# Kernel tuning notes

Measured on AMD Instinct MI355X. Metric: run time of the kernel, lower is better.

The kernel has to match this reference:

```python
import jax, jax.numpy as jnp
import numpy as np

B = 64; H = 64; W = 64; C = 128
NH = 4; WS = 4; SHIFT = 2
N = WS * WS; HD = C // NH; SCALE = HD ** -0.5
HID = 4 * C; EPS = 1e-6


def _rel_index():
    # faithful to source: meshgrid(coords_w, coords_h, indexing='ij'); hard-coded 4 == WS
    coords = np.stack(np.meshgrid(np.arange(WS), np.arange(WS), indexing='ij')).reshape(2, -1)
    rel = coords[:, :, None] - coords[:, None, :]
    rel = rel.transpose(1, 2, 0).copy()
    rel[:, :, 0] += WS - 1
    rel[:, :, 1] += WS - 1
    rel[:, :, 0] *= 2 * WS - 1
    return rel.sum(-1)  # (N, N) int

REL_IDX = jnp.asarray(_rel_index())


def _attn_mask():
    img = np.zeros((H, W))
    sl = (slice(0, -WS), slice(-WS, -SHIFT), slice(-SHIFT, None))
    cnt = 0
    for hs in sl:
        for ws_ in sl:
            img[hs, ws_] = cnt
            cnt += 1
    mw = img.reshape(H // WS, WS, W // WS, WS).transpose(0, 2, 1, 3).reshape(-1, N)
    m = mw[:, None, :] - mw[:, :, None]  # (nW, N, N)
    return jnp.asarray(np.where(m != 0, -100.0, 0.0).astype(np.float32))

MASK = _attn_mask()  # (nW, N, N)


def _ln(x, s, b):
    mu = x.mean(-1, keepdims=True)
    var = ((x - mu) ** 2).mean(-1, keepdims=True)
    return (x - mu) * jax.lax.rsqrt(var + EPS) * s + b


def setup_inputs() -> dict:
    key = jax.random.key(0)
    ks = jax.random.split(key, 8)
    def nrm(k, shape, scale=0.02):
        return jax.random.normal(k, shape, jnp.float32) * scale
    return dict(
        x=jax.random.normal(ks[0], (B, H * W, C), jnp.float32),
        ln1_scale=jnp.ones((C,), jnp.float32), ln1_bias=jnp.zeros((C,), jnp.float32),
        qkv_w=nrm(ks[1], (C, 3 * C)), qkv_b=jnp.zeros((3 * C,), jnp.float32),
        rel_bias=nrm(ks[2], ((2 * WS - 1) ** 2, NH)),
        proj_w=nrm(ks[3], (C, C)), proj_b=jnp.zeros((C,), jnp.float32),
        ln2_scale=jnp.ones((C,), jnp.float32), ln2_bias=jnp.zeros((C,), jnp.float32),
        fc1_w=nrm(ks[4], (C, HID)), fc1_b=jnp.zeros((HID,), jnp.float32),
        fc2_w=nrm(ks[5], (HID, C)), fc2_b=jnp.zeros((C,), jnp.float32),
    )


def reference(x, ln1_scale, ln1_bias, qkv_w, qkv_b, rel_bias, proj_w, proj_b,
              ln2_scale, ln2_bias, fc1_w, fc1_b, fc2_w, fc2_b):
    shortcut = x
    h = _ln(x, ln1_scale, ln1_bias).reshape(B, H, W, C)
    h = jnp.roll(h, (-SHIFT, -SHIFT), axis=(1, 2))
    # window partition -> (B*nW, N, C)
    xw = h.reshape(B, H // WS, WS, W // WS, WS, C).transpose(0, 1, 3, 2, 4, 5).reshape(-1, N, C)
    B_ = xw.shape[0]
    qkv = (xw @ qkv_w + qkv_b).reshape(B_, N, 3, NH, HD).transpose(2, 0, 3, 1, 4)
    q, k, v = qkv[0] * SCALE, qkv[1], qkv[2]
    attn = jnp.einsum('bhnd,bhmd->bhnm', q, k)  # (B_, NH, N, N)
    bias = rel_bias[REL_IDX.reshape(-1)].reshape(N, N, NH).transpose(2, 0, 1)
    attn = attn + bias[None]
    nW = MASK.shape[0]
    attn = attn.reshape(B_ // nW, nW, NH, N, N) + MASK[None, :, None]
    attn = jax.nn.softmax(attn.reshape(B_, NH, N, N), axis=-1)
    attn = jax.nn.softmax(attn, axis=-1)  # source applies softmax twice when mask is present
    out = jnp.einsum('bhnm,bhmd->bhnd', attn, v).transpose(0, 2, 1, 3).reshape(B_, N, C)
    out = out @ proj_w + proj_b
    # window reverse
    h = out.reshape(B, H // WS, W // WS, WS, WS, C).transpose(0, 1, 3, 2, 4, 5).reshape(B, H, W, C)
    h = jnp.roll(h, (SHIFT, SHIFT), axis=(1, 2)).reshape(B, H * W, C)
    x = shortcut + h
    m = _ln(x, ln2_scale, ln2_bias)
    m = jax.nn.gelu(m @ fc1_w + fc1_b) @ fc2_w + fc2_b  # flax nn.gelu default approximate=True
    return x + m
```

## Files before the change

### kernel.cpp

```cpp
#include <hip/hip_runtime.h>

typedef __bf16 bf16x8 __attribute__((ext_vector_type(8)));
typedef __bf16 bf16x4 __attribute__((ext_vector_type(4)));
typedef float f32x4 __attribute__((ext_vector_type(4)));
typedef unsigned short us8 __attribute__((ext_vector_type(8)));
typedef unsigned short us4 __attribute__((ext_vector_type(4)));
typedef short sh4 __attribute__((ext_vector_type(4)));

#define SCALE_Q 0.17677669529663687f

__device__ __forceinline__ unsigned short f2b(float f) {
    __bf16 h = (__bf16)f;
    return __builtin_bit_cast(unsigned short, h);
}
__device__ __forceinline__ float b2f(unsigned short h) {
    union { unsigned u; float f; } v; v.u = ((unsigned)h) << 16;
    return v.f;
}
__device__ __forceinline__ f32x4 mfma16(us8 a, us8 b, f32x4 c) {
    return __builtin_amdgcn_mfma_f32_16x16x32_bf16(
        __builtin_bit_cast(bf16x8, a), __builtin_bit_cast(bf16x8, b), c, 0, 0, 0);
}

#if __has_builtin(__builtin_amdgcn_mfma_f32_16x16x16bf16_1k)
__device__ __forceinline__ f32x4 mfma16k16(us4 a, us4 b, f32x4 c) {
    return __builtin_amdgcn_mfma_f32_16x16x16bf16_1k(
        __builtin_bit_cast(sh4, a), __builtin_bit_cast(sh4, b), c, 0, 0, 0);
}
#elif __has_builtin(__builtin_amdgcn_mfma_f32_16x16x16_bf16)
__device__ __forceinline__ f32x4 mfma16k16(us4 a, us4 b, f32x4 c) {
    return __builtin_amdgcn_mfma_f32_16x16x16_bf16(
        __builtin_bit_cast(bf16x4, a), __builtin_bit_cast(bf16x4, b), c, 0, 0, 0);
}
#else
__device__ __forceinline__ f32x4 mfma16k16(us4 a, us4 b, f32x4 c) {
    asm volatile("v_mfma_f32_16x16x16_bf16 %0, %1, %2, %0"
                 : "+v"(c) : "v"(a), "v"(b));
    return c;
}
#endif

__device__ __forceinline__ us8 lds_ld8(const unsigned short* base, int byteoff) {
    return *(const us8*)((const char*)base + byteoff);
}
__device__ __forceinline__ void lds_st8(unsigned short* base, int byteoff, us8 v) {
    *(us8*)((char*)base + byteoff) = v;
}

__global__ void k_pack_qkvw(const float* __restrict__ qkv_w, unsigned short* __restrict__ dst) {
    int gid = blockIdx.x * 256 + threadIdx.x;
    int blk = gid >> 9, rem = gid & 511;
    int lane = rem >> 3, j = rem & 7;
    int w = blk / 24, r1 = blk % 24, ct = r1 >> 2, kk = r1 & 3;
    int col = w * 96 + ct * 16 + (lane & 15);
    int k = kk * 32 + (lane >> 4) * 8 + j;
    float v = qkv_w[k * 384 + col];
    if (col < 128) v *= SCALE_Q;
    dst[gid] = f2b(v);
}
__global__ void k_scale_qkvb(const float* __restrict__ qkv_b, float* __restrict__ dst) {
    int i = blockIdx.x * 256 + threadIdx.x;
    if (i < 384) dst[i] = qkv_b[i] * (i < 128 ? SCALE_Q : 1.f);
}
__global__ void k_pack_projw(const float* __restrict__ proj_w, unsigned short* __restrict__ dst) {
    int gid = blockIdx.x * 256 + threadIdx.x;
    int blk = gid >> 9, rem = gid & 511;
    int lane = rem >> 3, j = rem & 7;
    int w = blk >> 3, r1 = blk & 7, ct = r1 >> 2, kk = r1 & 3;
    int col = w * 32 + ct * 16 + (lane & 15);
    int k = kk * 32 + (lane >> 4) * 8 + j;
    dst[gid] = f2b(proj_w[k * 128 + col]);
}

__global__ void k_pack_mlp(const float* __restrict__ fc1_w, const float* __restrict__ fc2_w,
                           unsigned short* __restrict__ wPack) {
    int gid = blockIdx.x * 256 + threadIdx.x;
    int pair = gid >> 13;
    int rem = gid & 8191;
    float v;
    if (rem < 4096) {
        int half = rem >> 11;
        int r2 = rem & 2047;
        int kk = r2 >> 9, r3 = r2 & 511;
        int lane = r3 >> 3, j = r3 & 7;
        int m = lane & 15;
        int col = pair * 32 + (m >> 2) * 8 + half * 4 + (m & 3);
        int k = kk * 32 + (lane >> 4) * 8 + j;
        v = fc1_w[(size_t)k * 512 + col];
    } else {
        int r2 = rem - 4096;
        int co = r2 >> 9, r3 = r2 & 511;
        int lane = r3 >> 3, j = r3 & 7;
        int k = pair * 32 + (lane >> 4) * 8 + j;
        v = fc2_w[(size_t)k * 128 + co * 16 + (lane & 15)];
    }
    wPack[gid] = f2b(v);
}

__global__ __launch_bounds__(256, 3) void k_block1(
    const float* __restrict__ x,
    const float* __restrict__ ln1s, const float* __restrict__ ln1b,
    const unsigned short* __restrict__ qkvWp, const float* __restrict__ qkvBs,
    const float* __restrict__ relb,
    const unsigned short* __restrict__ projWp, const float* __restrict__ projB,
    float* __restrict__ out)
{
    __shared__ unsigned short sm[4 * 6144];
    __shared__ float sbias[196];
    const int tid = threadIdx.x;
    const int wave = tid >> 6, lane = tid & 63;
    const int g = lane >> 4, m16 = lane & 15;
    if (tid < 196) sbias[tid] = relb[tid];
    const int win0 = blockIdx.x * 4;
    const int winM = win0 + wave;
    const int bbM = winM >> 8, whM = (winM >> 4) & 15, wnM = winM & 15;

    {
        float4 sc0 = *(const float4*)(ln1s + m16 * 8);
        float4 sc1 = *(const float4*)(ln1s + m16 * 8 + 4);
        float4 bi0 = *(const float4*)(ln1b + m16 * 8);
        float4 bi1 = *(const float4*)(ln1b + m16 * 8 + 4);
        #pragma unroll
        for (int it = 0; it < 4; ++it) {
            int tok = it * 4 + g;
            int ti = tok >> 2, tj = tok & 3;
            int hh = (whM * 4 + ti + 2) & 63, ww = (wnM * 4 + tj + 2) & 63;
            const float* xr = x + ((((size_t)bbM << 12) | (hh << 6) | ww) * 128) + m16 * 8;
            float4 v0 = *(const float4*)xr, v1 = *(const float4*)(xr + 4);
            float sum = v0.x + v0.y + v0.z + v0.w + v1.x + v1.y + v1.z + v1.w;
            float sq  = v0.x*v0.x + v0.y*v0.y + v0.z*v0.z + v0.w*v0.w
                      + v1.x*v1.x + v1.y*v1.y + v1.z*v1.z + v1.w*v1.w;
            #pragma unroll
            for (int m = 1; m < 16; m <<= 1) { sum += __shfl_xor(sum, m); sq += __shfl_xor(sq, m); }
            float mu = sum * 0.0078125f;
            float rstd = rsqrtf(sq * 0.0078125f - mu * mu + 1e-6f);
            us8 o;
            o[0] = f2b((v0.x - mu) * rstd * sc0.x + bi0.x);
            o[1] = f2b((v0.y - mu) * rstd * sc0.y + bi0.y);
            o[2] = f2b((v0.z - mu) * rstd * sc0.z + bi0.z);
            o[3] = f2b((v0.w - mu) * rstd * sc0.w + bi0.w);
            o[4] = f2b((v1.x - mu) * rstd * sc1.x + bi1.x);
            o[5] = f2b((v1.y - mu) * rstd * sc1.y + bi1.y);
            o[6] = f2b((v1.z - mu) * rstd * sc1.z + bi1.z);
            o[7] = f2b((v1.w - mu) * rstd * sc1.w + bi1.w);
            lds_st8(sm, wave * 12288 + tok * 256 + ((m16 * 16) ^ ((tok & 7) << 4)), o);
        }
    }
    __syncthreads();

    us8 afr[4][4];
    #pragma unroll
    for (int w = 0; w < 4; ++w)
        #pragma unroll
        for (int k = 0; k < 4; ++k)
            afr[w][k] = lds_ld8(sm, w * 12288 + m16 * 256 + ((k * 64 + g * 16) ^ ((m16 & 7) << 4)));
    __syncthreads();

    #pragma unroll
    for (int ct = 0; ct < 6; ++ct) {
        const unsigned short* bp = qkvWp + (size_t)((wave * 6 + ct) * 4) * 512 + lane * 8;
        us8 b0 = *(const us8*)(bp);
        us8 b1 = *(const us8*)(bp + 512);
        us8 b2 = *(const us8*)(bp + 1024);
        us8 b3 = *(const us8*)(bp + 1536);
        f32x4 acc[4] = {{0.f,0.f,0.f,0.f},{0.f,0.f,0.f,0.f},{0.f,0.f,0.f,0.f},{0.f,0.f,0.f,0.f}};
        #pragma unroll
        for (int w = 0; w < 4; ++w) {
            acc[w] = mfma16(afr[w][0], b0, acc[w]);
            acc[w] = mfma16(afr[w][1], b1, acc[w]);
            acc[w] = mfma16(afr[w][2], b2, acc[w]);
            acc[w] = mfma16(afr[w][3], b3, acc[w]);
        }
        const int c = wave * 96 + ct * 16 + m16;
        const float bias = qkvBs[c];
        const int s = c >> 7;
        const int rem = c & 127, hq = rem >> 5, hd = rem & 31;
        #pragma unroll
        for (int w = 0; w < 4; ++w) {
            const int base = w * 12288;
            if (s == 2) {
                us4 pk;
                #pragma unroll
                for (int jj = 0; jj < 4; ++jj) pk[jj] = f2b(acc[w][jj] + bias);
                *(us4*)((char*)sm + base + 8192 + hq * 1024 + hd * 32
                        + ((g ^ ((hd >> 2) & 3)) << 3)) = pk;
            } else {
                #pragma unroll
                for (int jj = 0; jj < 4; ++jj) {
                    int tok = g * 4 + jj;
                    int chunk = (hd >> 3) ^ ((tok >> 1) & 3);
                    *(unsigned short*)((char*)sm + base + s * 4096 + hq * 1024
                                       + tok * 64 + chunk * 16 + (hd & 7) * 2)
                        = f2b(acc[w][jj] + bias);
                }
            }
        }
    }
    __syncthreads();

    {
        const int base = wave * 12288;
        const int ti = m16 >> 2, tj = m16 & 3;
        const int hhq = whM * 4 + ti, wwq = wnM * 4 + tj;
        const int myid = (hhq < 60 ? 0 : (hhq < 62 ? 3 : 6)) + (wwq < 60 ? 0 : (wwq < 62 ? 1 : 2));
        const int qkswz = (g ^ ((m16 >> 1) & 3)) * 16;
        const int vswz  = (g ^ ((m16 >> 2) & 3)) << 3;
        f32x4 po[4][2];
        #pragma unroll
        for (int h = 0; h < 4; ++h) {
            us8 kf = lds_ld8(sm, base + 4096 + h * 1024 + m16 * 64 + qkswz);
            us8 qf = lds_ld8(sm, base +        h * 1024 + m16 * 64 + qkswz);
            f32x4 st = mfma16(kf, qf, (f32x4){0.f,0.f,0.f,0.f});
            float p[4];
            #pragma unroll
            for (int jj = 0; jj < 4; ++jj) {
                int kk = g * 4 + jj;
                int pi = kk >> 2, pj = kk & 3;
                int hhk = whM * 4 + pi, wwk = wnM * 4 + pj;
                int pid = (hhk < 60 ? 0 : (hhk < 62 ? 3 : 6)) + (wwk < 60 ? 0 : (wwk < 62 ? 1 : 2));
                float v = st[jj] + sbias[((ti - pi + 3) * 7 + (tj - pj + 3)) * 4 + h];
                p[jj] = (pid != myid) ? v - 100.f : v;
            }
            #pragma unroll
            for (int rep = 0; rep < 2; ++rep) {
                float mx = fmaxf(fmaxf(p[0], p[1]), fmaxf(p[2], p[3]));
                mx = fmaxf(mx, __shfl_xor(mx, 16));
                mx = fmaxf(mx, __shfl_xor(mx, 32));
                float ssum = 0.f;
                #pragma unroll
                for (int jj = 0; jj < 4; ++jj) { p[jj] = __expf(p[jj] - mx); ssum += p[jj]; }
                ssum += __shfl_xor(ssum, 16);
                ssum += __shfl_xor(ssum, 32);
                float inv = 1.f / ssum;
                #pragma unroll
                for (int jj = 0; jj < 4; ++jj) p[jj] *= inv;
            }
            us4 pf;
            #pragma unroll
            for (int jj = 0; jj < 4; ++jj) pf[jj] = f2b(p[jj]);
            #pragma unroll
            for (int dh = 0; dh < 2; ++dh) {
                us4 vf = *(const us4*)((const char*)sm + base + 8192 + h * 1024
                                       + (dh * 16 + m16) * 32 + vswz);
                po[h][dh] = mfma16k16(vf, pf, (f32x4){0.f,0.f,0.f,0.f});
            }
        }
        #pragma unroll
        for (int h = 0; h < 4; ++h)
            #pragma unroll
            for (int dh = 0; dh < 2; ++dh) {
                us4 pk;
                #pragma unroll
                for (int jj = 0; jj < 4; ++jj) pk[jj] = f2b(po[h][dh][jj]);
                *(us4*)((char*)sm + base + m16 * 256
                        + ((h * 64 + dh * 32 + g * 8) ^ ((m16 & 7) << 4))) = pk;
            }
    }
    __syncthreads();

    {
        us8 cfr[4][4];
        #pragma unroll
        for (int w = 0; w < 4; ++w)
            #pragma unroll
            for (int k = 0; k < 4; ++k)
                cfr[w][k] = lds_ld8(sm, w * 12288 + m16 * 256 + ((k * 64 + g * 16) ^ ((m16 & 7) << 4)));
        #pragma unroll
        for (int ct = 0; ct < 2; ++ct) {
            const unsigned short* bp = projWp + (size_t)((wave * 2 + ct) * 4) * 512 + lane * 8;
            us8 b0 = *(const us8*)(bp);
            us8 b1 = *(const us8*)(bp + 512);
            us8 b2 = *(const us8*)(bp + 1024);
            us8 b3 = *(const us8*)(bp + 1536);
            const int c = wave * 32 + ct * 16 + m16;
            const float pb = projB[c];
            #pragma unroll
            for (int w = 0; w < 4; ++w) {
                f32x4 acc = {0.f, 0.f, 0.f, 0.f};
                acc = mfma16(cfr[w][0], b0, acc);
                acc = mfma16(cfr[w][1], b1, acc);
                acc = mfma16(cfr[w][2], b2, acc);
                acc = mfma16(cfr[w][3], b3, acc);
                const int winw = win0 + w;
                const int bb = winw >> 8, wh = (winw >> 4) & 15, wn = winw & 15;
                #pragma unroll
                for (int jj = 0; jj < 4; ++jj) {
                    int tok = g * 4 + jj;
                    int hh3 = (wh * 4 + (tok >> 2) + 2) & 63;
                    int ww3 = (wn * 4 + (tok & 3) + 2) & 63;
                    size_t t = (((size_t)bb << 12) | (hh3 << 6) | ww3);
                    out[t * 128 + c] = acc[jj] + pb + x[t * 128 + c];
                }
            }
        }
    }
}

__global__ __launch_bounds__(512, 4) void k_block2(
    float* __restrict__ out,
    const float* __restrict__ ln2s, const float* __restrict__ ln2b,
    const unsigned short* __restrict__ wPack,
    const float* __restrict__ fc1B, const float* __restrict__ fc2B)
{
    __shared__ unsigned short smem[16384];
    const int tid = threadIdx.x;
    const int wave = tid >> 6, lane = tid & 63;
    const int g = lane >> 4, m16 = lane & 15;
    const size_t r0 = (size_t)blockIdx.x * 128;
    unsigned short* scr = &smem[wave * 2048];

    {
        float4 sc0 = *(const float4*)(ln2s + m16 * 8);
        float4 sc1 = *(const float4*)(ln2s + m16 * 8 + 4);
        float4 bi0 = *(const float4*)(ln2b + m16 * 8);
        float4 bi1 = *(const float4*)(ln2b + m16 * 8 + 4);
        #pragma unroll
        for (int it = 0; it < 4; ++it) {
            int lr = it * 4 + g;
            const float* xr = out + (r0 + wave * 16 + lr) * 128 + m16 * 8;
            float4 v0 = *(const float4*)xr, v1 = *(const float4*)(xr + 4);
            float sum = v0.x + v0.y + v0.z + v0.w + v1.x + v1.y + v1.z + v1.w;
            float sq  = v0.x*v0.x + v0.y*v0.y + v0.z*v0.z + v0.w*v0.w
                      + v1.x*v1.x + v1.y*v1.y + v1.z*v1.z + v1.w*v1.w;
            #pragma unroll
            for (int m = 1; m < 16; m <<= 1) { sum += __shfl_xor(sum, m); sq += __shfl_xor(sq, m); }
            float mu = sum * 0.0078125f;
            float rstd = rsqrtf(sq * 0.0078125f - mu * mu + 1e-6f);
            us8 o;
            o[0] = f2b((v0.x - mu) * rstd * sc0.x + bi0.x);
            o[1] = f2b((v0.y - mu) * rstd * sc0.y + bi0.y);
            o[2] = f2b((v0.z - mu) * rstd * sc0.z + bi0.z);
            o[3] = f2b((v0.w - mu) * rstd * sc0.w + bi0.w);
            o[4] = f2b((v1.x - mu) * rstd * sc1.x + bi1.x);
            o[5] = f2b((v1.y - mu) * rstd * sc1.y + bi1.y);
            o[6] = f2b((v1.z - mu) * rstd * sc1.z + bi1.z);
            o[7] = f2b((v1.w - mu) * rstd * sc1.w + bi1.w);
            lds_st8(scr, lr * 256 + ((m16 * 16) ^ ((lr & 7) << 4)), o);
        }
    }
    us8 bx[4];
    #pragma unroll
    for (int kk = 0; kk < 4; ++kk)
        bx[kk] = lds_ld8(scr, m16 * 256 + ((kk * 64 + g * 16) ^ ((m16 & 7) << 4)));
    __syncthreads();

    #pragma unroll
    for (int sub = 0; sub < 2; ++sub) {
        const unsigned short* src = wPack + sub * 4096 + tid * 8;
        unsigned short* dst = &smem[sub * 4096 + wave * 512];
#if __has_builtin(__builtin_amdgcn_global_load_lds)
        __builtin_amdgcn_global_load_lds(
            (const __attribute__((address_space(1))) void*)src,
            (__attribute__((address_space(3))) void*)dst, 16, 0, 0);
#else
        *(us8*)(dst + lane * 8) = *(const us8*)src;
#endif
    }
    __syncthreads();

    f32x4 accO[8];
    #pragma unroll
    for (int co = 0; co < 8; ++co) accO[co] = (f32x4){0.f, 0.f, 0.f, 0.f};

    for (int p = 0; p < 16; ++p) {
        if (p < 15) {
            #pragma unroll
            for (int sub = 0; sub < 2; ++sub) {
                const unsigned short* src = wPack + (p + 1) * 8192 + sub * 4096 + tid * 8;
                unsigned short* dst = &smem[((p + 1) & 1) * 8192 + sub * 4096 + wave * 512];
#if __has_builtin(__builtin_amdgcn_global_load_lds)
                __builtin_amdgcn_global_load_lds(
                    (const __attribute__((address_space(1))) void*)src,
                    (__attribute__((address_space(3))) void*)dst, 16, 0, 0);
#else
                *(us8*)(dst + lane * 8) = *(const us8*)src;
#endif
            }
        }
        const char* wb = (const char*)&smem[(p & 1) * 8192];
        f32x4 hA = {0.f, 0.f, 0.f, 0.f};
        hA = mfma16(*(const us8*)(wb +    0 + lane * 16), bx[0], hA);
        hA = mfma16(*(const us8*)(wb + 1024 + lane * 16), bx[1], hA);
        hA = mfma16(*(const us8*)(wb + 2048 + lane * 16), bx[2], hA);
        hA = mfma16(*(const us8*)(wb + 3072 + lane * 16), bx[3], hA);
        f32x4 hB = {0.f, 0.f, 0.f, 0.f};
        hB = mfma16(*(const us8*)(wb + 4096 + lane * 16), bx[0], hB);
        hB = mfma16(*(const us8*)(wb + 5120 + lane * 16), bx[1], hB);
        hB = mfma16(*(const us8*)(wb + 6144 + lane * 16), bx[2], hB);
        hB = mfma16(*(const us8*)(wb + 7168 + lane * 16), bx[3], hB);
        float4 bA = *(const float4*)(fc1B + p * 32 + g * 8);
        float4 bB = *(const float4*)(fc1B + p * 32 + g * 8 + 4);
        us8 pa;
        #pragma unroll
        for (int jj = 0; jj < 4; ++jj) {
            float v = hA[jj] + ((const float*)&bA)[jj];
            float z = v + 0.044715f * v * v * v;
            float e = __builtin_amdgcn_exp2f(-2.3022082f * z);
            pa[jj] = f2b(v * __builtin_amdgcn_rcpf(1.f + e));
            float w = hB[jj] + ((const float*)&bB)[jj];
            float z2 = w + 0.044715f * w * w * w;
            float e2 = __builtin_amdgcn_exp2f(-2.3022082f * z2);
            pa[4 + jj] = f2b(w * __builtin_amdgcn_rcpf(1.f + e2));
        }
        #pragma unroll
        for (int co = 0; co < 8; ++co) {
            us8 bw = *(const us8*)(wb + 8192 + co * 1024 + lane * 16);
            accO[co] = mfma16(pa, bw, accO[co]);
        }
        __syncthreads();
    }

    #pragma unroll
    for (int co = 0; co < 8; ++co) {
        int col = co * 16 + m16;
        float b2v = fc2B[col];
        #pragma unroll
        for (int jj = 0; jj < 4; ++jj) {
            size_t row = r0 + wave * 16 + g * 4 + jj;
            float* op = out + row * 128 + col;
            *op = accO[co][jj] + b2v + *op;
        }
    }
}

extern "C" void kernel_launch(void* const* d_in, const int* in_sizes, int n_in,
                              void* d_out, int out_size, void* d_ws, size_t ws_size,
                              hipStream_t stream) {
    const float* x        = (const float*)d_in[0];
    const float* ln1_s    = (const float*)d_in[1];
    const float* ln1_b    = (const float*)d_in[2];
    const float* qkv_w    = (const float*)d_in[3];
    const float* qkv_b    = (const float*)d_in[4];
    const float* rel_bias = (const float*)d_in[5];
    const float* proj_w   = (const float*)d_in[6];
    const float* proj_b   = (const float*)d_in[7];
    const float* ln2_s    = (const float*)d_in[8];
    const float* ln2_b    = (const float*)d_in[9];
    const float* fc1_w    = (const float*)d_in[10];
    const float* fc1_b    = (const float*)d_in[11];
    const float* fc2_w    = (const float*)d_in[12];
    const float* fc2_b    = (const float*)d_in[13];
    float* out = (float*)d_out;
    char* ws = (char*)d_ws;

    unsigned short* qkv_wp  = (unsigned short*)(ws);
    unsigned short* proj_wp = (unsigned short*)(ws + 98304);
    unsigned short* wpack   = (unsigned short*)(ws + 131072);
    float*          qkv_bs  = (float*)(ws + 393216);

    k_pack_qkvw<<<192, 256, 0, stream>>>(qkv_w, qkv_wp);
    k_scale_qkvb<<<2, 256, 0, stream>>>(qkv_b, qkv_bs);
    k_pack_projw<<<64, 256, 0, stream>>>(proj_w, proj_wp);
    k_pack_mlp<<<512, 256, 0, stream>>>(fc1_w, fc2_w, wpack);

    k_block1<<<4096, 256, 0, stream>>>(x, ln1_s, ln1_b, qkv_wp, qkv_bs, rel_bias,
                                       proj_wp, proj_b, out);
    k_block2<<<2048, 512, 0, stream>>>(out, ln2_s, ln2_b, wpack, fc1_b, fc2_b);
}
```

Baseline: 223.5 us.

## Give each MLP wave two row tiles so weight LDS loads are reused

The MLP kernel now runs 4 waves per block instead of 8, and each wave handles 32 rows, two 16-row tiles, rather than 16. Each fc1/fc2 weight fragment read from LDS now feeds two MFMAs, halving LDS weight traffic per FLOP. The first weight chunk's load is issued before LayerNorm so the global-to-LDS copy overlaps with it. In exchange each wave holds twice the accumulators and activations, so register pressure rises. The launch bounds are lowered to 3 blocks of 256 threads, which with 48KB of LDS per block can reduce occupancy.

New measurement: 216.5 us. 3.2% less time.

```diff
diff --git a/kernel.cpp b/kernel.cpp
--- a/kernel.cpp
+++ b/kernel.cpp
@@ -296,28 +296,43 @@
     }
 }
 
-__global__ __launch_bounds__(512, 4) void k_block2(
+__global__ __launch_bounds__(256, 3) void k_block2(
     float* __restrict__ out,
     const float* __restrict__ ln2s, const float* __restrict__ ln2b,
     const unsigned short* __restrict__ wPack,
     const float* __restrict__ fc1B, const float* __restrict__ fc2B)
 {
-    __shared__ unsigned short smem[16384];
+    __shared__ unsigned short smem[24576];
     const int tid = threadIdx.x;
     const int wave = tid >> 6, lane = tid & 63;
     const int g = lane >> 4, m16 = lane & 15;
     const size_t r0 = (size_t)blockIdx.x * 128;
     unsigned short* scr = &smem[wave * 2048];
 
-    {
-        float4 sc0 = *(const float4*)(ln2s + m16 * 8);
-        float4 sc1 = *(const float4*)(ln2s + m16 * 8 + 4);
-        float4 bi0 = *(const float4*)(ln2b + m16 * 8);
-        float4 bi1 = *(const float4*)(ln2b + m16 * 8 + 4);
+    #pragma unroll
+    for (int sub = 0; sub < 4; ++sub) {
+        const unsigned short* src = wPack + sub * 2048 + tid * 8;
+        unsigned short* dst = &smem[8192 + sub * 2048 + wave * 512];
+#if __has_builtin(__builtin_amdgcn_global_load_lds)
+        __builtin_amdgcn_global_load_lds(
+            (const __attribute__((address_space(1))) void*)src,
+            (__attribute__((address_space(3))) void*)dst, 16, 0, 0);
+#else
+        *(us8*)(dst + lane * 8) = *(const us8*)src;
+#endif
+    }
+
+    float4 sc0 = *(const float4*)(ln2s + m16 * 8);
+    float4 sc1 = *(const float4*)(ln2s + m16 * 8 + 4);
+    float4 bi0 = *(const float4*)(ln2b + m16 * 8);
+    float4 bi1 = *(const float4*)(ln2b + m16 * 8 + 4);
+    us8 bx[2][4];
+    #pragma unroll
+    for (int rt = 0; rt < 2; ++rt) {
         #pragma unroll
         for (int it = 0; it < 4; ++it) {
             int lr = it * 4 + g;
-            const float* xr = out + (r0 + wave * 16 + lr) * 128 + m16 * 8;
+            const float* xr = out + (r0 + wave * 32 + rt * 16 + lr) * 128 + m16 * 8;
             float4 v0 = *(const float4*)xr, v1 = *(const float4*)(xr + 4);
             float sum = v0.x + v0.y + v0.z + v0.w + v1.x + v1.y + v1.z + v1.w;
             float sq  = v0.x*v0.x + v0.y*v0.y + v0.z*v0.z + v0.w*v0.w
@@ -337,37 +352,24 @@
             o[7] = f2b((v1.w - mu) * rstd * sc1.w + bi1.w);
             lds_st8(scr, lr * 256 + ((m16 * 16) ^ ((lr & 7) << 4)), o);
         }
-    }
-    us8 bx[4];
-    #pragma unroll
-    for (int kk = 0; kk < 4; ++kk)
-        bx[kk] = lds_ld8(scr, m16 * 256 + ((kk * 64 + g * 16) ^ ((m16 & 7) << 4)));
+        #pragma unroll
+        for (int kk = 0; kk < 4; ++kk)
+            bx[rt][kk] = lds_ld8(scr, m16 * 256 + ((kk * 64 + g * 16) ^ ((m16 & 7) << 4)));
+    }
     __syncthreads();
 
-    #pragma unroll
-    for (int sub = 0; sub < 2; ++sub) {
-        const unsigned short* src = wPack + sub * 4096 + tid * 8;
-        unsigned short* dst = &smem[sub * 4096 + wave * 512];
-#if __has_builtin(__builtin_amdgcn_global_load_lds)
-        __builtin_amdgcn_global_load_lds(
-            (const __attribute__((address_space(1))) void*)src,
-            (__attribute__((address_space(3))) void*)dst, 16, 0, 0);
-#else
-        *(us8*)(dst + lane * 8) = *(const us8*)src;
-#endif
-    }
-    __syncthreads();
-
-    f32x4 accO[8];
-    #pragma unroll
-    for (int co = 0; co < 8; ++co) accO[co] = (f32x4){0.f, 0.f, 0.f, 0.f};
+    f32x4 accO[2][8];
+    #pragma unroll
+    for (int rt = 0; rt < 2; ++rt)
+        #pragma unroll
+        for (int co = 0; co < 8; ++co) accO[rt][co] = (f32x4){0.f, 0.f, 0.f, 0.f};
 
     for (int p = 0; p < 16; ++p) {
         if (p < 15) {
             #pragma unroll
-            for (int sub = 0; sub < 2; ++sub) {
-                const unsigned short* src = wPack + (p + 1) * 8192 + sub * 4096 + tid * 8;
-                unsigned short* dst = &smem[((p + 1) & 1) * 8192 + sub * 4096 + wave * 512];
+            for (int sub = 0; sub < 4; ++sub) {
+                const unsigned short* src = wPack + (p + 1) * 8192 + sub * 2048 + tid * 8;
+                unsigned short* dst = &smem[8192 + ((p + 1) & 1) * 8192 + sub * 2048 + wave * 512];
 #if __has_builtin(__builtin_amdgcn_global_load_lds)
                 __builtin_amdgcn_global_load_lds(
                     (const __attribute__((address_space(1))) void*)src,
@@ -377,50 +379,61 @@
 #endif
             }
         }
-        const char* wb = (const char*)&smem[(p & 1) * 8192];
-        f32x4 hA = {0.f, 0.f, 0.f, 0.f};
-        hA = mfma16(*(const us8*)(wb +    0 + lane * 16), bx[0], hA);
-        hA = mfma16(*(const us8*)(wb + 1024 + lane * 16), bx[1], hA);
-        hA = mfma16(*(const us8*)(wb + 2048 + lane * 16), bx[2], hA);
-        hA = mfma16(*(const us8*)(wb + 3072 + lane * 16), bx[3], hA);
-        f32x4 hB = {0.f, 0.f, 0.f, 0.f};
-        hB = mfma16(*(const us8*)(wb + 4096 + lane * 16), bx[0], hB);
-        hB = mfma16(*(const us8*)(wb + 5120 + lane * 16), bx[1], hB);
-        hB = mfma16(*(const us8*)(wb + 6144 + lane * 16), bx[2], hB);
-        hB = mfma16(*(const us8*)(wb + 7168 + lane * 16), bx[3], hB);
+        const char* wb = (const char*)&smem[8192 + (p & 1) * 8192];
+        f32x4 hA0 = {0.f,0.f,0.f,0.f}, hA1 = {0.f,0.f,0.f,0.f};
+        #pragma unroll
+        for (int kk = 0; kk < 4; ++kk) {
+            us8 aw = *(const us8*)(wb + kk * 1024 + lane * 16);
+            hA0 = mfma16(aw, bx[0][kk], hA0);
+            hA1 = mfma16(aw, bx[1][kk], hA1);
+        }
+        f32x4 hB0 = {0.f,0.f,0.f,0.f}, hB1 = {0.f,0.f,0.f,0.f};
+        #pragma unroll
+        for (int kk = 0; kk < 4; ++kk) {
+            us8 aw = *(const us8*)(wb + 4096 + kk * 1024 + lane * 16);
+            hB0 = mfma16(aw, bx[0][kk], hB0);
+            hB1 = mfma16(aw, bx[1][kk], hB1);
+        }
         float4 bA = *(const float4*)(fc1B + p * 32 + g * 8);
         float4 bB = *(const float4*)(fc1B + p * 32 + g * 8 + 4);
-        us8 pa;
+        us8 pa0, pa1;
         #pragma unroll
         for (int jj = 0; jj < 4; ++jj) {
-            float v = hA[jj] + ((const float*)&bA)[jj];
-            float z = v + 0.044715f * v * v * v;
-            float e = __builtin_amdgcn_exp2f(-2.3022082f * z);
-            pa[jj] = f2b(v * __builtin_amdgcn_rcpf(1.f + e));
-            float w = hB[jj] + ((const float*)&bB)[jj];
-            float z2 = w + 0.044715f * w * w * w;
-            float e2 = __builtin_amdgcn_exp2f(-2.3022082f * z2);
-            pa[4 + jj] = f2b(w * __builtin_amdgcn_rcpf(1.f + e2));
+            float v0 = hA0[jj] + ((const float*)&bA)[jj];
+            float z0 = v0 + 0.044715f * v0 * v0 * v0;
+            pa0[jj] = f2b(v0 * __builtin_amdgcn_rcpf(1.f + __builtin_amdgcn_exp2f(-2.3022082f * z0)));
+            float w0 = hB0[jj] + ((const float*)&bB)[jj];
+            float y0 = w0 + 0.044715f * w0 * w0 * w0;
+            pa0[4 + jj] = f2b(w0 * __builtin_amdgcn_rcpf(1.f + __builtin_amdgcn_exp2f(-2.3022082f * y0)));
+            float v1 = hA1[jj] + ((const float*)&bA)[jj];
+            float z1 = v1 + 0.044715f * v1 * v1 * v1;
+            pa1[jj] = f2b(v1 * __builtin_amdgcn_rcpf(1.f + __builtin_amdgcn_exp2f(-2.3022082f * z1)));
+            float w1 = hB1[jj] + ((const float*)&bB)[jj];
+            float y1 = w1 + 0.044715f * w1 * w1 * w1;
+            pa1[4 + jj] = f2b(w1 * __builtin_amdgcn_rcpf(1.f + __builtin_amdgcn_exp2f(-2.3022082f * y1)));
         }
         #pragma unroll
         for (int co = 0; co < 8; ++co) {
             us8 bw = *(const us8*)(wb + 8192 + co * 1024 + lane * 16);
-            accO[co] = mfma16(pa, bw, accO[co]);
+            accO[0][co] = mfma16(pa0, bw, accO[0][co]);
+            accO[1][co] = mfma16(pa1, bw, accO[1][co]);
         }
         __syncthreads();
     }
 
     #pragma unroll
-    for (int co = 0; co < 8; ++co) {
-        int col = co * 16 + m16;
-        float b2v = fc2B[col];
-        #pragma unroll
-        for (int jj = 0; jj < 4; ++jj) {
-            size_t row = r0 + wave * 16 + g * 4 + jj;
-            float* op = out + row * 128 + col;
-            *op = accO[co][jj] + b2v + *op;
-        }
-    }
+    for (int rt = 0; rt < 2; ++rt)
+        #pragma unroll
+        for (int co = 0; co < 8; ++co) {
+            int col = co * 16 + m16;
+            float b2v = fc2B[col];
+            #pragma unroll
+            for (int jj = 0; jj < 4; ++jj) {
+                size_t row = r0 + wave * 32 + rt * 16 + g * 4 + jj;
+                float* op = out + row * 128 + col;
+                *op = accO[rt][co][jj] + b2v + *op;
+            }
+        }
 }
 
 extern "C" void kernel_launch(void* const* d_in, const int* in_sizes, int n_in,
@@ -455,5 +468,5 @@
 
     k_block1<<<4096, 256, 0, stream>>>(x, ln1_s, ln1_b, qkv_wp, qkv_bs, rel_bias,
                                        proj_wp, proj_b, out);
-    k_block2<<<2048, 512, 0, stream>>>(out, ln2_s, ln2_b, wpack, fc1_b, fc2_b);
-}
+    k_block2<<<2048, 256, 0, stream>>>(out, ln2_s, ln2_b, wpack, fc1_b, fc2_b);
+}
```

## Fuse attention block and MLP block into one kernel via LDS handoff

Applied to the files above, without the earlier changes.

Merges the attention/projection kernel and the LN2+MLP kernel into a single kernel. The post-attention residual stays in shared memory, so it is no longer written to global memory and read back by a second kernel. The cost is a larger shared-memory footprint, launch bounds lowered from 3 to 2 blocks, and MLP weight streaming now done per 64-token block (256 threads) instead of per 128-token block. That doubles the total weight loads from global or L2 and may reduce occupancy.

After: 267.2 us. +19.5%, slower.

```diff
diff --git a/kernel.cpp b/kernel.cpp
--- a/kernel.cpp
+++ b/kernel.cpp
@@ -97,16 +97,20 @@
     wPack[gid] = f2b(v);
 }
 
-__global__ __launch_bounds__(256, 3) void k_block1(
+__global__ __launch_bounds__(256, 2) void k_fused(
     const float* __restrict__ x,
     const float* __restrict__ ln1s, const float* __restrict__ ln1b,
     const unsigned short* __restrict__ qkvWp, const float* __restrict__ qkvBs,
     const float* __restrict__ relb,
     const unsigned short* __restrict__ projWp, const float* __restrict__ projB,
+    const float* __restrict__ ln2s, const float* __restrict__ ln2b,
+    const unsigned short* __restrict__ wPack,
+    const float* __restrict__ fc1B, const float* __restrict__ fc2B,
     float* __restrict__ out)
 {
-    __shared__ unsigned short sm[4 * 6144];
+    __shared__ unsigned short smem[32768];
     __shared__ float sbias[196];
+    unsigned short* sm = smem;
     const int tid = threadIdx.x;
     const int wave = tid >> 6, lane = tid & 63;
     const int g = lane >> 4, m16 = lane & 15;
@@ -265,6 +269,7 @@
             #pragma unroll
             for (int k = 0; k < 4; ++k)
                 cfr[w][k] = lds_ld8(sm, w * 12288 + m16 * 256 + ((k * 64 + g * 16) ^ ((m16 & 7) << 4)));
+        __syncthreads();
         #pragma unroll
         for (int ct = 0; ct < 2; ++ct) {
             const unsigned short* bp = projWp + (size_t)((wave * 2 + ct) * 4) * 512 + lane * 8;
@@ -289,26 +294,16 @@
                     int hh3 = (wh * 4 + (tok >> 2) + 2) & 63;
                     int ww3 = (wn * 4 + (tok & 3) + 2) & 63;
                     size_t t = (((size_t)bb << 12) | (hh3 << 6) | ww3);
-                    out[t * 128 + c] = acc[jj] + pb + x[t * 128 + c];
+                    float xm = acc[jj] + pb + x[t * 128 + c];
+                    *(float*)((char*)smem + (w * 16 + tok) * 512
+                              + ((c * 4) ^ ((tok & 7) << 4))) = xm;
                 }
             }
         }
     }
-}
-
-__global__ __launch_bounds__(512, 4) void k_block2(
-    float* __restrict__ out,
-    const float* __restrict__ ln2s, const float* __restrict__ ln2b,
-    const unsigned short* __restrict__ wPack,
-    const float* __restrict__ fc1B, const float* __restrict__ fc2B)
-{
-    __shared__ unsigned short smem[16384];
-    const int tid = threadIdx.x;
-    const int wave = tid >> 6, lane = tid & 63;
-    const int g = lane >> 4, m16 = lane & 15;
-    const size_t r0 = (size_t)blockIdx.x * 128;
-    unsigned short* scr = &smem[wave * 2048];
-
+    __syncthreads();
+
+    unsigned short* scr = (unsigned short*)((char*)smem + 32768 + wave * 4096);
     {
         float4 sc0 = *(const float4*)(ln2s + m16 * 8);
         float4 sc1 = *(const float4*)(ln2s + m16 * 8 + 4);
@@ -316,9 +311,11 @@
         float4 bi1 = *(const float4*)(ln2b + m16 * 8 + 4);
         #pragma unroll
         for (int it = 0; it < 4; ++it) {
-            int lr = it * 4 + g;
-            const float* xr = out + (r0 + wave * 16 + lr) * 128 + m16 * 8;
-            float4 v0 = *(const float4*)xr, v1 = *(const float4*)(xr + 4);
+            int r = it * 4 + g;
+            const char* xmrow = (const char*)smem + (wave * 16 + r) * 512;
+            int swz = (r & 7) << 4;
+            float4 v0 = *(const float4*)(xmrow + ((m16 * 32) ^ swz));
+            float4 v1 = *(const float4*)(xmrow + ((m16 * 32 + 16) ^ swz));
             float sum = v0.x + v0.y + v0.z + v0.w + v1.x + v1.y + v1.z + v1.w;
             float sq  = v0.x*v0.x + v0.y*v0.y + v0.z*v0.z + v0.w*v0.w
                       + v1.x*v1.x + v1.y*v1.y + v1.z*v1.z + v1.w*v1.w;
@@ -335,7 +332,7 @@
             o[5] = f2b((v1.y - mu) * rstd * sc1.y + bi1.y);
             o[6] = f2b((v1.z - mu) * rstd * sc1.z + bi1.z);
             o[7] = f2b((v1.w - mu) * rstd * sc1.w + bi1.w);
-            lds_st8(scr, lr * 256 + ((m16 * 16) ^ ((lr & 7) << 4)), o);
+            lds_st8(scr, r * 256 + ((m16 * 16) ^ ((r & 7) << 4)), o);
         }
     }
     us8 bx[4];
@@ -345,9 +342,9 @@
     __syncthreads();
 
     #pragma unroll
-    for (int sub = 0; sub < 2; ++sub) {
-        const unsigned short* src = wPack + sub * 4096 + tid * 8;
-        unsigned short* dst = &smem[sub * 4096 + wave * 512];
+    for (int sub = 0; sub < 4; ++sub) {
+        const unsigned short* src = wPack + sub * 2048 + tid * 8;
+        unsigned short* dst = &smem[16384 + sub * 2048 + wave * 512];
 #if __has_builtin(__builtin_amdgcn_global_load_lds)
         __builtin_amdgcn_global_load_lds(
             (const __attribute__((address_space(1))) void*)src,
@@ -365,9 +362,9 @@
     for (int p = 0; p < 16; ++p) {
         if (p < 15) {
             #pragma unroll
-            for (int sub = 0; sub < 2; ++sub) {
-                const unsigned short* src = wPack + (p + 1) * 8192 + sub * 4096 + tid * 8;
-                unsigned short* dst = &smem[((p + 1) & 1) * 8192 + sub * 4096 + wave * 512];
+            for (int sub = 0; sub < 4; ++sub) {
+                const unsigned short* src = wPack + (p + 1) * 8192 + sub * 2048 + tid * 8;
+                unsigned short* dst = &smem[16384 + ((p + 1) & 1) * 8192 + sub * 2048 + wave * 512];
 #if __has_builtin(__builtin_amdgcn_global_load_lds)
                 __builtin_amdgcn_global_load_lds(
                     (const __attribute__((address_space(1))) void*)src,
@@ -377,17 +374,13 @@
 #endif
             }
         }
-        const char* wb = (const char*)&smem[(p & 1) * 8192];
-        f32x4 hA = {0.f, 0.f, 0.f, 0.f};
-        hA = mfma16(*(const us8*)(wb +    0 + lane * 16), bx[0], hA);
-        hA = mfma16(*(const us8*)(wb + 1024 + lane * 16), bx[1], hA);
-        hA = mfma16(*(const us8*)(wb + 2048 + lane * 16), bx[2], hA);
-        hA = mfma16(*(const us8*)(wb + 3072 + lane * 16), bx[3], hA);
-        f32x4 hB = {0.f, 0.f, 0.f, 0.f};
-        hB = mfma16(*(const us8*)(wb + 4096 + lane * 16), bx[0], hB);
-        hB = mfma16(*(const us8*)(wb + 5120 + lane * 16), bx[1], hB);
-        hB = mfma16(*(const us8*)(wb + 6144 + lane * 16), bx[2], hB);
-        hB = mfma16(*(const us8*)(wb + 7168 + lane * 16), bx[3], hB);
+        const char* wb = (const char*)&smem[16384 + (p & 1) * 8192];
+        f32x4 hA = {0.f, 0.f, 0.f, 0.f}, hB = {0.f, 0.f, 0.f, 0.f};
+        #pragma unroll
+        for (int kk = 0; kk < 4; ++kk) {
+            hA = mfma16(*(const us8*)(wb + kk * 1024 + lane * 16), bx[kk], hA);
+            hB = mfma16(*(const us8*)(wb + 4096 + kk * 1024 + lane * 16), bx[kk], hB);
+        }
         float4 bA = *(const float4*)(fc1B + p * 32 + g * 8);
         float4 bB = *(const float4*)(fc1B + p * 32 + g * 8 + 4);
         us8 pa;
@@ -395,12 +388,10 @@
         for (int jj = 0; jj < 4; ++jj) {
             float v = hA[jj] + ((const float*)&bA)[jj];
             float z = v + 0.044715f * v * v * v;
-            float e = __builtin_amdgcn_exp2f(-2.3022082f * z);
-            pa[jj] = f2b(v * __builtin_amdgcn_rcpf(1.f + e));
+            pa[jj] = f2b(v * __builtin_amdgcn_rcpf(1.f + __builtin_amdgcn_exp2f(-2.3022082f * z)));
             float w = hB[jj] + ((const float*)&bB)[jj];
-            float z2 = w + 0.044715f * w * w * w;
-            float e2 = __builtin_amdgcn_exp2f(-2.3022082f * z2);
-            pa[4 + jj] = f2b(w * __builtin_amdgcn_rcpf(1.f + e2));
+            float y = w + 0.044715f * w * w * w;
+            pa[4 + jj] = f2b(w * __builtin_amdgcn_rcpf(1.f + __builtin_amdgcn_exp2f(-2.3022082f * y)));
         }
         #pragma unroll
         for (int co = 0; co < 8; ++co) {
@@ -410,15 +401,23 @@
         __syncthreads();
     }
 
-    #pragma unroll
-    for (int co = 0; co < 8; ++co) {
-        int col = co * 16 + m16;
-        float b2v = fc2B[col];
-        #pragma unroll
-        for (int jj = 0; jj < 4; ++jj) {
-            size_t row = r0 + wave * 16 + g * 4 + jj;
-            float* op = out + row * 128 + col;
-            *op = accO[co][jj] + b2v + *op;
+    {
+        const int winw = win0 + wave;
+        const int bb = winw >> 8, wh = (winw >> 4) & 15, wn = winw & 15;
+        #pragma unroll
+        for (int co = 0; co < 8; ++co) {
+            int col = co * 16 + m16;
+            float b2v = fc2B[col];
+            #pragma unroll
+            for (int jj = 0; jj < 4; ++jj) {
+                int tok = g * 4 + jj;
+                float xm = *(const float*)((const char*)smem + (wave * 16 + tok) * 512
+                                           + ((col * 4) ^ ((tok & 7) << 4)));
+                int hh3 = (wh * 4 + (tok >> 2) + 2) & 63;
+                int ww3 = (wn * 4 + (tok & 3) + 2) & 63;
+                size_t t = (((size_t)bb << 12) | (hh3 << 6) | ww3);
+                out[t * 128 + col] = accO[co][jj] + b2v + xm;
+            }
         }
     }
 }
@@ -453,7 +452,7 @@
     k_pack_projw<<<64, 256, 0, stream>>>(proj_w, proj_wp);
     k_pack_mlp<<<512, 256, 0, stream>>>(fc1_w, fc2_w, wpack);
 
-    k_block1<<<4096, 256, 0, stream>>>(x, ln1_s, ln1_b, qkv_wp, qkv_bs, rel_bias,
-                                       proj_wp, proj_b, out);
-    k_block2<<<2048, 512, 0, stream>>>(out, ln2_s, ln2_b, wpack, fc1_b, fc2_b);
-}
+    k_fused<<<4096, 256, 0, stream>>>(x, ln1_s, ln1_b, qkv_wp, qkv_bs, rel_bias,
+                                      proj_wp, proj_b, ln2_s, ln2_b, wpack,
+                                      fc1_b, fc2_b, out);
+}
```
